# Kernel optimization log

Hardware: AMD Instinct MI355X
Metric: run time of the kernel (lower is better)

## Reference

```python
import jax, jax.numpy as jnp
import numpy as np
from jax import lax

B, C, L, H = 32, 256, 1280, 5
D = L // H  # head dim = 256
EPS = 1e-5


def setup_inputs() -> dict:
    key = jax.random.key(0)
    ks = jax.random.split(key, 16)
    s = 0.02
    inp = {
        "x": jax.random.normal(ks[0], (B, C, L), jnp.float32),
        # rank encoder Linear(L, L)
        "re_w": jax.random.normal(ks[1], (L, L), jnp.float32) * s,
        "re_b": jnp.zeros((L,), jnp.float32),
        # layer norms
        "ln1_g": jnp.ones((L,), jnp.float32), "ln1_b": jnp.zeros((L,), jnp.float32),
        "ln2_g": jnp.ones((L,), jnp.float32), "ln2_b": jnp.zeros((L,), jnp.float32),
        # attention projections (stored [in, out]; y @ W + b)
        "wq": jax.random.normal(ks[2], (L, L), jnp.float32) * s, "bq": jnp.zeros((L,), jnp.float32),
        "wk": jax.random.normal(ks[3], (L, L), jnp.float32) * s, "bk": jnp.zeros((L,), jnp.float32),
        "wv": jax.random.normal(ks[4], (L, L), jnp.float32) * s, "bv": jnp.zeros((L,), jnp.float32),
        "wo": jax.random.normal(ks[5], (L, L), jnp.float32) * s, "bo": jnp.zeros((L,), jnp.float32),
        # FFN (ffn_size == hidden_size == L in this module)
        "ffn_w1": jax.random.normal(ks[6], (L, L), jnp.float32) * s, "ffn_b1": jnp.zeros((L,), jnp.float32),
        "ffn_w2": jax.random.normal(ks[7], (L, L), jnp.float32) * s, "ffn_b2": jnp.zeros((L,), jnp.float32),
        # Conv1d(C, C, k=3, stride=1, pad=1, bias=False) + BatchNorm1d (eval) + ReLU
        "conv_w": jax.random.normal(ks[8], (C, C, 3), jnp.float32) * (2.0 / (C * 3)) ** 0.5,
        "bn_g": jnp.ones((C,), jnp.float32), "bn_b": jnp.zeros((C,), jnp.float32),
        "bn_m": jnp.zeros((C,), jnp.float32), "bn_v": jnp.ones((C,), jnp.float32),
    }
    return inp


def _layernorm(t, g, b):
    m = jnp.mean(t, axis=-1, keepdims=True)
    v = jnp.var(t, axis=-1, keepdims=True)
    return (t - m) * lax.rsqrt(v + EPS) * g + b


def reference(x, re_w, re_b, ln1_g, ln1_b, ln2_g, ln2_b,
              wq, bq, wk, bk, wv, bv, wo, bo,
              ffn_w1, ffn_b1, ffn_w2, ffn_b2,
              conv_w, bn_g, bn_b, bn_m, bn_v):
    b_, c_, l_ = x.shape
    # _getrank_: rank from double argsort (descending), mapped to (L - rank)/L
    rank_i = jnp.argsort(jnp.argsort(-x, axis=-1), axis=-1)
    rank = (l_ - rank_i).astype(x.dtype) / l_
    node = x + rank @ re_w + re_b                      # [B, C, L]

    # EncoderLayer: pre-LN MHSA (attn_bias is None in this call path)
    y = _layernorm(node, ln1_g, ln1_b)
    scale = D ** -0.5
    q = (y @ wq + bq).reshape(b_, c_, H, D).transpose(0, 2, 1, 3) * scale  # [B,H,C,D]
    k = (y @ wk + bk).reshape(b_, c_, H, D).transpose(0, 2, 1, 3)
    v = (y @ wv + bv).reshape(b_, c_, H, D).transpose(0, 2, 1, 3)
    attn = jax.nn.softmax(jnp.einsum('bhqd,bhkd->bhqk', q, k), axis=-1)   # [B,H,C,C]
    o = jnp.einsum('bhqk,bhkd->bhqd', attn, v)
    o = o.transpose(0, 2, 1, 3).reshape(b_, c_, l_) @ wo + bo
    h = node + o  # dropout is identity in eval

    # FFN sublayer
    y2 = _layernorm(h, ln2_g, ln2_b)
    f = jax.nn.gelu(y2 @ ffn_w1 + ffn_b1, approximate=False) @ ffn_w2 + ffn_b2
    h = h + f                                           # [B, C, L]

    # ConvBNRelu: Conv1d(k=3, s=1, p=1, no bias) -> BN (eval stats) -> ReLU
    conv = lax.conv_general_dilated(h, conv_w, window_strides=(1,),
                                    padding=[(1, 1)],
                                    dimension_numbers=('NCH', 'OIH', 'NCH'))
    bn = (conv - bn_m[None, :, None]) * lax.rsqrt(bn_v[None, :, None] + EPS)
    bn = bn * bn_g[None, :, None] + bn_b[None, :, None]
    return jax.nn.relu(bn)
```

## Files before the change

kernel.cpp:

```cpp
#include <hip/hip_runtime.h>
#include <hip/hip_bf16.h>
#include <stdint.h>

#define L_   1280
#define B_   32
#define C_   256
#define H_   5
#define D_   256
#define BC_  8192
#define EPSV 1e-5f

typedef __attribute__((ext_vector_type(8))) short bf16x8;
typedef __attribute__((ext_vector_type(4))) float f32x4;
typedef __hip_bfloat16 bf16;

__device__ __forceinline__ bf16 f2bf(float v) { return __float2bfloat16(v); }
__device__ __forceinline__ float bf2f(bf16 v) { return __bfloat162float(v); }

#define GLDS16(gptr, lptr)                                                        \
    __builtin_amdgcn_global_load_lds(                                             \
        (const __attribute__((address_space(1))) void*)(gptr),                    \
        (__attribute__((address_space(3))) void*)(lptr), 16, 0, 0)

struct WtArgs { const float* src[7]; bf16* dst[7]; };

__global__ __launch_bounds__(256) void transpose7(WtArgs a) {
    const int mat = blockIdx.z;
    const float* src = a.src[mat];
    bf16* dst = a.dst[mat];
    __shared__ float tile[32][33];
    const int bx = blockIdx.x * 32;
    const int by = blockIdx.y * 32;
    const int tx = threadIdx.x, ty = threadIdx.y;
    #pragma unroll
    for (int r = ty; r < 32; r += 8)
        tile[r][tx] = src[(size_t)(by + r) * L_ + bx + tx];
    __syncthreads();
    #pragma unroll
    for (int r = ty; r < 32; r += 8)
        dst[(size_t)(bx + r) * L_ + by + tx] = f2bf(tile[tx][r]);
}

__global__ __launch_bounds__(256) void prep_conv(const float* cw, const float* g, const float* b,
                                                 const float* m, const float* v,
                                                 bf16* WT, float* sc, float* bi) {
    const int i = blockIdx.x * 256 + threadIdx.x;
    if (i < 3 * 256 * 256) {
        const int co = i / 768;
        const int r = i - co * 768;
        const int t = r >> 8, ci = r & 255;
        WT[i] = f2bf(cw[(co * 256 + ci) * 3 + t]);
    }
    if (i < 256) {
        const float s = g[i] * rsqrtf(v[i] + EPSV);
        sc[i] = s;
        bi[i] = b[i] - m[i] * s;
    }
}

__global__ __launch_bounds__(256) void rank_kernel(const float* __restrict__ x, bf16* __restrict__ R) {
    __shared__ float vals[L_];
    __shared__ float sv[L_];
    __shared__ int hist[256];
    __shared__ int pfx[256];
    __shared__ int cur[256];
    const int row = blockIdx.x, tid = threadIdx.x;
    const float* src = x + (size_t)row * L_;
    for (int i = tid; i < L_; i += 256) vals[i] = src[i];
    hist[tid] = 0;
    __syncthreads();
    float myv[5]; int myb[5];
    #pragma unroll
    for (int ii = 0; ii < 5; ii++) {
        const float v = vals[tid + ii * 256];
        int bk = (int)((4.0f - v) * 32.0f);
        bk = bk < 0 ? 0 : (bk > 255 ? 255 : bk);
        myv[ii] = v; myb[ii] = bk;
        atomicAdd(&hist[bk], 1);
    }
    __syncthreads();
    pfx[tid] = hist[tid];
    __syncthreads();
    for (int off = 1; off < 256; off <<= 1) {
        int t = (tid >= off) ? pfx[tid - off] : 0;
        __syncthreads();
        pfx[tid] += t;
        __syncthreads();
    }
    cur[tid] = pfx[tid] - hist[tid];
    __syncthreads();
    #pragma unroll
    for (int ii = 0; ii < 5; ii++) {
        const int pos = atomicAdd(&cur[myb[ii]], 1);
        sv[pos] = myv[ii];
    }
    __syncthreads();
    #pragma unroll
    for (int ii = 0; ii < 5; ii++) {
        const int bk = myb[ii]; const float v = myv[ii];
        const int s = pfx[bk] - hist[bk], e = pfx[bk];
        int cg = s;
        for (int p = s; p < e; p++) cg += (sv[p] > v) ? 1 : 0;
        R[(size_t)row * L_ + tid + ii * 256] = f2bf((float)(L_ - cg) * (1.0f / L_));
    }
}

__global__ __launch_bounds__(256) void ln_kernel(const bf16* __restrict__ in,
                                                 const float* __restrict__ g,
                                                 const float* __restrict__ b,
                                                 bf16* __restrict__ out) {
    const int row = blockIdx.x, tid = threadIdx.x;
    const bf16* src = in + (size_t)row * L_;
    uint2 ra = ((const uint2*)src)[tid];
    bf16 a4[4]; *(uint2*)a4 = ra;
    const float a0 = bf2f(a4[0]), a1 = bf2f(a4[1]), a2 = bf2f(a4[2]), a3 = bf2f(a4[3]);
    float s = a0 + a1 + a2 + a3;
    float ss = a0 * a0 + a1 * a1 + a2 * a2 + a3 * a3;
    float b0 = 0, b1 = 0, b2 = 0, b3 = 0;
    if (tid < 64) {
        uint2 rb = ((const uint2*)src)[256 + tid];
        bf16 b4[4]; *(uint2*)b4 = rb;
        b0 = bf2f(b4[0]); b1 = bf2f(b4[1]); b2 = bf2f(b4[2]); b3 = bf2f(b4[3]);
        s += b0 + b1 + b2 + b3;
        ss += b0 * b0 + b1 * b1 + b2 * b2 + b3 * b3;
    }
    #pragma unroll
    for (int off = 32; off > 0; off >>= 1) {
        s += __shfl_down(s, off, 64);
        ss += __shfl_down(ss, off, 64);
    }
    __shared__ float rs[4], rss[4];
    __shared__ float mean_s, rstd_s;
    if ((tid & 63) == 0) { rs[tid >> 6] = s; rss[tid >> 6] = ss; }
    __syncthreads();
    if (tid == 0) {
        const float S = rs[0] + rs[1] + rs[2] + rs[3];
        const float SS = rss[0] + rss[1] + rss[2] + rss[3];
        const float m = S * (1.0f / L_);
        const float var = SS * (1.0f / L_) - m * m;
        mean_s = m; rstd_s = rsqrtf(var + EPSV);
    }
    __syncthreads();
    const float m = mean_s, r = rstd_s;
    {
        const int c = tid * 4;
        bf16 t4[4];
        t4[0] = f2bf((a0 - m) * r * g[c + 0] + b[c + 0]);
        t4[1] = f2bf((a1 - m) * r * g[c + 1] + b[c + 1]);
        t4[2] = f2bf((a2 - m) * r * g[c + 2] + b[c + 2]);
        t4[3] = f2bf((a3 - m) * r * g[c + 3] + b[c + 3]);
        *(uint2*)(out + (size_t)row * L_ + c) = *(uint2*)t4;
    }
    if (tid < 64) {
        const int c = 1024 + tid * 4;
        bf16 t4[4];
        t4[0] = f2bf((b0 - m) * r * g[c + 0] + b[c + 0]);
        t4[1] = f2bf((b1 - m) * r * g[c + 1] + b[c + 1]);
        t4[2] = f2bf((b2 - m) * r * g[c + 2] + b[c + 2]);
        t4[3] = f2bf((b3 - m) * r * g[c + 3] + b[c + 3]);
        *(uint2*)(out + (size_t)row * L_ + c) = *(uint2*)t4;
    }
}

__global__ __launch_bounds__(256) void softmax_kernel(const bf16* __restrict__ S, bf16* __restrict__ P) {
    const int row = blockIdx.x * 4 + (threadIdx.x >> 6);
    const int l = threadIdx.x & 63;
    const bf16* src = S + (size_t)row * 256 + l * 4;
    uint2 raw = *(const uint2*)src;
    bf16 s4[4]; *(uint2*)s4 = raw;
    float v0 = bf2f(s4[0]), v1 = bf2f(s4[1]);
    float v2 = bf2f(s4[2]), v3 = bf2f(s4[3]);
    float mx = fmaxf(fmaxf(v0, v1), fmaxf(v2, v3));
    #pragma unroll
    for (int off = 1; off < 64; off <<= 1) mx = fmaxf(mx, __shfl_xor(mx, off, 64));
    const float e0 = expf(v0 - mx), e1 = expf(v1 - mx), e2 = expf(v2 - mx), e3 = expf(v3 - mx);
    float sm = e0 + e1 + e2 + e3;
    #pragma unroll
    for (int off = 1; off < 64; off <<= 1) sm += __shfl_xor(sm, off, 64);
    const float inv = 1.0f / sm;
    bf16 t4[4] = { f2bf(e0 * inv), f2bf(e1 * inv), f2bf(e2 * inv), f2bf(e3 * inv) };
    *(uint2*)(P + (size_t)row * 256 + l * 4) = *(uint2*)t4;
}

__global__ __launch_bounds__(256) void zero_pads(bf16* h2T) {
    const int i = blockIdx.x * 256 + threadIdx.x;
    const int b = i >> 9;
    const int which = (i >> 8) & 1;
    const int ci = i & 255;
    const long row = which ? 1281 : 0;
    h2T[(long)b * (1282 * 256) + row * 256 + ci] = f2bf(0.0f);
}

struct GemmP {
    const bf16* A;  long lda, sA1, sA2;
    const bf16* Bt; long ldb, sB1, sB2;
    int zmod;
    int K;
    float* outF; bf16* outB; bf16* outB2; bf16* outB3; long ldc, sC1, sC2;
    const float* bias; const float* bias2; const float* bias3;
    const float* res; const bf16* resB; long ldres, sR1, sR2;
    const float* rowscale; const float* rowbias;
    float scale;
};

constexpr int E_NODE = 0;
constexpr int E_HRES = 1;
constexpr int E_BF16 = 5;
constexpr int E_GELU = 6;
constexpr int E_FFN2T = 7;
constexpr int E_CONVBNR = 8;
constexpr int E_QKV = 9;

template <int EPI>
__global__ __launch_bounds__(256) void gemm_bt(GemmP p) {
    const int nwg  = gridDim.x * gridDim.y * gridDim.z;
    const int orig = (blockIdx.z * gridDim.y + blockIdx.y) * gridDim.x + blockIdx.x;
    int bx, rowg;
    if ((nwg & 7) == 0) {
        const int chunk = nwg >> 3;
        const int xcd = orig & 7, pos = orig >> 3;
        const int rpc = chunk / gridDim.x;
        if (rpc * gridDim.x == chunk) {
            bx   = pos / rpc;
            rowg = xcd * rpc + (pos - bx * rpc);
        } else {
            const int wgid = xcd * chunk + pos;
            bx = wgid % gridDim.x; rowg = wgid / gridDim.x;
        }
    } else {
        bx = blockIdx.x; rowg = blockIdx.z * gridDim.y + blockIdx.y;
    }
    const int by = rowg % gridDim.y;
    const int bz = rowg / gridDim.y;

    const int zq = bz / p.zmod, zr = bz % p.zmod;
    const bf16* A  = p.A  + (long)zq * p.sA1 + (long)zr * p.sA2;
    const bf16* Bt = p.Bt + (long)zq * p.sB1 + (long)zr * p.sB2;
    const int row0 = by * 128, col0 = bx * 128;

    __shared__ __align__(16) bf16 shm[24576];

    const int tid = threadIdx.x;
    const int l = tid & 63, w = tid >> 6;
    const int wr = w >> 1, wc = w & 1;

    f32x4 acc[4][4];
    #pragma unroll
    for (int m = 0; m < 4; m++)
        #pragma unroll
        for (int n = 0; n < 4; n++)
            acc[m][n] = (f32x4){0.f, 0.f, 0.f, 0.f};

    const bf16* gA = A  + (long)(row0 + w * 16 + (l >> 2)) * p.lda + (l & 3) * 8;
    const bf16* gB = Bt + (long)(col0 + w * 16 + (l >> 2)) * p.ldb + (l & 3) * 8;
    const long aStep = 64 * p.lda, bStep = 64 * p.ldb;

    auto STAGE = [&](int buf) {
        bf16* lA = shm + buf * 4096;
        bf16* lB = shm + 12288 + buf * 4096;
        GLDS16(gA,         lA + w * 512);
        GLDS16(gA + aStep, lA + 2048 + w * 512);
        GLDS16(gB,         lB + w * 512);
        GLDS16(gB + bStep, lB + 2048 + w * 512);
        gA += 32; gB += 32;
    };
    auto COMPUTE = [&](int buf) {
        const bf16* lA = shm + buf * 4096;
        const bf16* lB = shm + 12288 + buf * 4096;
        bf16x8 aF[4], bF[4];
        #pragma unroll
        for (int m = 0; m < 4; m++)
            aF[m] = *(const bf16x8*)(lA + (wr * 64 + m * 16 + (l & 15)) * 32 + (l >> 4) * 8);
        #pragma unroll
        for (int n = 0; n < 4; n++)
            bF[n] = *(const bf16x8*)(lB + (wc * 64 + n * 16 + (l & 15)) * 32 + (l >> 4) * 8);
        #pragma unroll
        for (int m = 0; m < 4; m++)
            #pragma unroll
            for (int n = 0; n < 4; n++)
                acc[m][n] = __builtin_amdgcn_mfma_f32_16x16x32_bf16(aF[m], bF[n], acc[m][n], 0, 0, 0);
    };

    const int nt = p.K >> 5;
    STAGE(0); STAGE(1);
    int cb = 0, sb = 2;
    for (int t = 0; t < nt - 1; ++t) {
        asm volatile("s_waitcnt vmcnt(4)" ::: "memory");
        __builtin_amdgcn_sched_barrier(0);
        __builtin_amdgcn_s_barrier();
        if (t + 2 < nt) STAGE(sb);
        COMPUTE(cb);
        cb = (cb == 2) ? 0 : cb + 1;
        sb = (sb == 2) ? 0 : sb + 1;
    }
    asm volatile("s_waitcnt vmcnt(0)" ::: "memory");
    __builtin_amdgcn_sched_barrier(0);
    __builtin_amdgcn_s_barrier();
    COMPUTE(cb);

    if constexpr (EPI == E_QKV) {
        if (col0 >= 2560) {
            const int v0  = col0 - 2560;
            const int hh  = v0 >> 8;
            const int dd0 = v0 & 255;
            const int b_  = row0 >> 8;
            const int c0b = row0 & 255;
            __syncthreads();
            #pragma unroll
            for (int m = 0; m < 4; m++)
                #pragma unroll
                for (int n = 0; n < 4; n++) {
                    const int cc = wc * 64 + n * 16 + (l & 15);
                    const float bb = p.bias3[v0 + cc];
                    #pragma unroll
                    for (int j = 0; j < 4; j++) {
                        const int r = wr * 64 + m * 16 + (l >> 4) * 4 + j;
                        shm[cc * 128 + (r ^ ((cc & 7) << 3))] = f2bf(acc[m][n][j] + bb);
                    }
                }
            __syncthreads();
            const int d = tid >> 1, ch = (tid & 1) * 64;
            bf16* dstRow = p.outB3 +
                (((long)((b_ * H_ + hh) * 256 + dd0 + d)) << 8) + c0b;
            #pragma unroll
            for (int g = 0; g < 8; g++) {
                const int rb = ch + g * 8;
                *(bf16x8*)(dstRow + rb) =
                    *(const bf16x8*)&shm[d * 128 + (rb ^ ((d & 7) << 3))];
            }
            return;
        }
    }

    const long cz = (long)zq * p.sC1 + (long)zr * p.sC2;
    const long rz = (long)zq * p.sR1 + (long)zr * p.sR2;
    #pragma unroll
    for (int m = 0; m < 4; m++) {
        #pragma unroll
        for (int n = 0; n < 4; n++) {
            const int gcol = col0 + wc * 64 + n * 16 + (l & 15);
            #pragma unroll
            for (int j = 0; j < 4; j++) {
                const int grow = row0 + wr * 64 + m * 16 + (l >> 4) * 4 + j;
                const float v = acc[m][n][j];
                if constexpr (EPI == E_NODE) {
                    p.outB[cz + (long)grow * p.ldc + gcol] =
                        f2bf(v + p.bias[gcol] + p.res[rz + (long)grow * p.ldres + gcol]);
                } else if constexpr (EPI == E_HRES) {
                    p.outB[cz + (long)grow * p.ldc + gcol] =
                        f2bf(v + p.bias[gcol] + bf2f(p.resB[rz + (long)grow * p.ldres + gcol]));
                } else if constexpr (EPI == E_BF16) {
                    p.outB[cz + (long)grow * p.ldc + gcol] = f2bf(v);
                } else if constexpr (EPI == E_GELU) {
                    const float t = v + p.bias[gcol];
                    p.outB[cz + (long)grow * p.ldc + gcol] =
                        f2bf(0.5f * t * (1.0f + erff(t * 0.70710678f)));
                } else if constexpr (EPI == E_FFN2T) {
                    const float t = v + p.bias[gcol] +
                                    bf2f(p.resB[rz + (long)grow * p.ldres + gcol]);
                    const int b_ = grow >> 8, ci = grow & 255;
                    p.outB[(long)b_ * (1282 * 256) + (long)(gcol + 1) * 256 + ci] = f2bf(t);
                } else if constexpr (EPI == E_CONVBNR) {
                    const float t = v * p.rowscale[grow] + p.rowbias[grow];
                    p.outF[cz + (long)grow * p.ldc + gcol] = fmaxf(t, 0.0f);
                } else if constexpr (EPI == E_QKV) {
                    if (gcol < 1280) {
                        p.outB[(long)grow * L_ + gcol] = f2bf((v + p.bias[gcol]) * p.scale);
                    } else {
                        const int c2 = gcol - 1280;
                        p.outB2[(long)grow * L_ + c2] = f2bf(v + p.bias2[c2]);
                    }
                }
            }
        }
    }
}

extern "C" void kernel_launch(void* const* d_in, const int* in_sizes, int n_in,
                              void* d_out, int out_size, void* d_ws, size_t ws_size,
                              hipStream_t stream) {
    const float* x    = (const float*)d_in[0];
    const float* re_w = (const float*)d_in[1];
    const float* re_b = (const float*)d_in[2];
    const float* ln1g = (const float*)d_in[3];
    const float* ln1b = (const float*)d_in[4];
    const float* ln2g = (const float*)d_in[5];
    const float* ln2b = (const float*)d_in[6];
    const float* wq   = (const float*)d_in[7];
    const float* bq   = (const float*)d_in[8];
    const float* wk   = (const float*)d_in[9];
    const float* bk   = (const float*)d_in[10];
    const float* wv   = (const float*)d_in[11];
    const float* bv   = (const float*)d_in[12];
    const float* wo   = (const float*)d_in[13];
    const float* bo   = (const float*)d_in[14];
    const float* fw1  = (const float*)d_in[15];
    const float* fb1  = (const float*)d_in[16];
    const float* fw2  = (const float*)d_in[17];
    const float* fb2  = (const float*)d_in[18];
    const float* convw = (const float*)d_in[19];
    const float* bng  = (const float*)d_in[20];
    const float* bnb  = (const float*)d_in[21];
    const float* bnm  = (const float*)d_in[22];
    const float* bnv  = (const float*)d_in[23];
    float* out = (float*)d_out;

    char* ws = (char*)d_ws;
    const size_t SZ_WT     = (size_t)L_ * L_ * 2;
    const size_t SZ_ACT_BF = (size_t)BC_ * L_ * 2;
    const size_t SZ_H2T    = (size_t)B_ * 1282 * 256 * 2;
    const size_t SZ_S      = (size_t)160 * 256 * 256 * 4;

    size_t off = 0;
    bf16* Wt[7];
    for (int i = 0; i < 7; i++) { Wt[i] = (bf16*)(ws + off); off += SZ_WT; }
    bf16* WconvT   = (bf16*)(ws + off); off += 393216;
    float* bnscale = (float*)(ws + off); off += 1024;
    float* bnbias  = (float*)(ws + off); off += 1024;
    bf16* RP  = (bf16*)(ws + off); off += SZ_ACT_BF;
    bf16* Yb  = (bf16*)(ws + off); off += SZ_ACT_BF;
    bf16* Qb  = (bf16*)(ws + off); off += SZ_ACT_BF;
    bf16* Kb  = (bf16*)(ws + off); off += SZ_H2T;
    float* Sb = (float*)(ws + off); off += SZ_S;
    bf16* nodeB = (bf16*)(ws + off); off += SZ_ACT_BF;
    bf16* Sbf = (bf16*)Sb;
    bf16* VT  = Sbf + (size_t)160 * 65536;
    (void)in_sizes; (void)n_in; (void)out_size;

    if (ws_size < off) return;

    WtArgs wa;
    wa.src[0] = re_w; wa.src[1] = wq; wa.src[2] = wk; wa.src[3] = wv;
    wa.src[4] = wo;  wa.src[5] = fw1; wa.src[6] = fw2;
    for (int i = 0; i < 7; i++) wa.dst[i] = Wt[i];
    transpose7<<<dim3(40, 40, 7), dim3(32, 8), 0, stream>>>(wa);
    prep_conv<<<dim3(768), 256, 0, stream>>>(convw, bng, bnb, bnm, bnv, WconvT, bnscale, bnbias);

    rank_kernel<<<dim3(BC_), 256, 0, stream>>>(x, RP);

    const dim3 gBig(L_ / 128, BC_ / 128, 1);
    const dim3 gQKV(3840 / 128, BC_ / 128, 1);
    const dim3 gAttn(2, 2, 160);
    const dim3 blk(256);

    {
        GemmP p{}; p.zmod = 1; p.K = L_;
        p.A = RP; p.lda = L_; p.Bt = Wt[0]; p.ldb = L_;
        p.outB = nodeB; p.ldc = L_; p.bias = re_b; p.res = x; p.ldres = L_;
        gemm_bt<E_NODE><<<gBig, blk, 0, stream>>>(p);
    }
    ln_kernel<<<dim3(BC_), blk, 0, stream>>>(nodeB, ln1g, ln1b, Yb);
    {
        GemmP p{}; p.zmod = 1; p.K = L_;
        p.A = Yb; p.lda = L_; p.Bt = Wt[1]; p.ldb = L_;
        p.outB = Qb; p.outB2 = Kb; p.outB3 = VT;
        p.bias = bq; p.bias2 = bk; p.bias3 = bv; p.scale = 0.0625f;
        gemm_bt<E_QKV><<<gQKV, blk, 0, stream>>>(p);
    }
    {
        GemmP p{}; p.zmod = H_; p.K = 256;
        p.A = Qb;  p.lda = L_; p.sA1 = (long)C_ * L_; p.sA2 = 256;
        p.Bt = Kb; p.ldb = L_; p.sB1 = (long)C_ * L_; p.sB2 = 256;
        p.outB = Sbf; p.ldc = 256; p.sC1 = (long)H_ * 65536; p.sC2 = 65536;
        gemm_bt<E_BF16><<<gAttn, blk, 0, stream>>>(p);
    }
    softmax_kernel<<<dim3(160 * 256 / 4), blk, 0, stream>>>(Sbf, RP);
    {
        GemmP p{}; p.zmod = H_; p.K = 256;
        p.A = RP;  p.lda = 256; p.sA1 = (long)H_ * 65536; p.sA2 = 65536;
        p.Bt = VT; p.ldb = 256; p.sB1 = (long)H_ * 65536; p.sB2 = 65536;
        p.outB = Qb; p.ldc = L_; p.sC1 = (long)C_ * L_; p.sC2 = 256;
        gemm_bt<E_BF16><<<gAttn, blk, 0, stream>>>(p);
    }
    {
        GemmP p{}; p.zmod = 1; p.K = L_;
        p.A = Qb; p.lda = L_; p.Bt = Wt[4]; p.ldb = L_;
        p.outB = nodeB; p.ldc = L_; p.bias = bo; p.resB = nodeB; p.ldres = L_;
        gemm_bt<E_HRES><<<gBig, blk, 0, stream>>>(p);
    }
    ln_kernel<<<dim3(BC_), blk, 0, stream>>>(nodeB, ln2g, ln2b, RP);
    {
        GemmP p{}; p.zmod = 1; p.K = L_;
        p.A = RP; p.lda = L_; p.Bt = Wt[5]; p.ldb = L_;
        p.outB = Yb; p.ldc = L_; p.bias = fb1;
        gemm_bt<E_GELU><<<gBig, blk, 0, stream>>>(p);
    }
    zero_pads<<<dim3(64), blk, 0, stream>>>(Kb);
    {
        GemmP p{}; p.zmod = 1; p.K = L_;
        p.A = Yb; p.lda = L_; p.Bt = Wt[6]; p.ldb = L_;
        p.outB = Kb; p.bias = fb2; p.resB = nodeB; p.ldres = L_;
        gemm_bt<E_FFN2T><<<gBig, blk, 0, stream>>>(p);
    }
    {
        GemmP p{}; p.zmod = 1; p.K = 768;
        p.A = WconvT; p.lda = 768;
        p.Bt = Kb; p.ldb = 256; p.sB1 = 1282 * 256;
        p.outF = out; p.ldc = L_; p.sC1 = (long)C_ * L_;
        p.rowscale = bnscale; p.rowbias = bnbias;
        gemm_bt<E_CONVBNR><<<dim3(L_ / 128, 2, B_), blk, 0, stream>>>(p);
    }
}
```

Baseline: 520.4 us.

## Enlarge GEMM tile to 256x128 and write V-transpose directly from registers

Doubles the M dimension of the shared GEMM block tile from 128 to 256 rows, with each wave now computing 128x64. This raises arithmetic intensity and halves the B-operand reloads, and the grids for all launches are halved in y to match. The LDS-staged transposed V epilogue is replaced with direct 8-byte stores from accumulators, removing a shared-memory round trip at the cost of less coalesced writes. The change doubles accumulator registers and raises LDS use, which may lower occupancy, and it halves the block count, which may under-fill the CUs on smaller launches such as attention and conv.

```diff
diff --git a/kernel.cpp b/kernel.cpp
--- a/kernel.cpp
+++ b/kernel.cpp
@@ -236,46 +236,47 @@
     const int zq = bz / p.zmod, zr = bz % p.zmod;
     const bf16* A  = p.A  + (long)zq * p.sA1 + (long)zr * p.sA2;
     const bf16* Bt = p.Bt + (long)zq * p.sB1 + (long)zr * p.sB2;
-    const int row0 = by * 128, col0 = bx * 128;
-
-    __shared__ __align__(16) bf16 shm[24576];
+    const int row0 = by * 256, col0 = bx * 128;
+
+    __shared__ __align__(16) bf16 shm[36864];
 
     const int tid = threadIdx.x;
     const int l = tid & 63, w = tid >> 6;
     const int wr = w >> 1, wc = w & 1;
 
-    f32x4 acc[4][4];
-    #pragma unroll
-    for (int m = 0; m < 4; m++)
+    f32x4 acc[8][4];
+    #pragma unroll
+    for (int m = 0; m < 8; m++)
         #pragma unroll
         for (int n = 0; n < 4; n++)
             acc[m][n] = (f32x4){0.f, 0.f, 0.f, 0.f};
 
     const bf16* gA = A  + (long)(row0 + w * 16 + (l >> 2)) * p.lda + (l & 3) * 8;
     const bf16* gB = Bt + (long)(col0 + w * 16 + (l >> 2)) * p.ldb + (l & 3) * 8;
-    const long aStep = 64 * p.lda, bStep = 64 * p.ldb;
 
     auto STAGE = [&](int buf) {
-        bf16* lA = shm + buf * 4096;
-        bf16* lB = shm + 12288 + buf * 4096;
-        GLDS16(gA,         lA + w * 512);
-        GLDS16(gA + aStep, lA + 2048 + w * 512);
-        GLDS16(gB,         lB + w * 512);
-        GLDS16(gB + bStep, lB + 2048 + w * 512);
+        bf16* lA = shm + buf * 8192;
+        bf16* lB = shm + 24576 + buf * 4096;
+        GLDS16(gA,                 lA + w * 512);
+        GLDS16(gA +  64 * p.lda,   lA + 2048 + w * 512);
+        GLDS16(gA + 128 * p.lda,   lA + 4096 + w * 512);
+        GLDS16(gA + 192 * p.lda,   lA + 6144 + w * 512);
+        GLDS16(gB,                 lB + w * 512);
+        GLDS16(gB +  64 * p.ldb,   lB + 2048 + w * 512);
         gA += 32; gB += 32;
     };
     auto COMPUTE = [&](int buf) {
-        const bf16* lA = shm + buf * 4096;
-        const bf16* lB = shm + 12288 + buf * 4096;
-        bf16x8 aF[4], bF[4];
+        const bf16* lA = shm + buf * 8192;
+        const bf16* lB = shm + 24576 + buf * 4096;
+        bf16x8 aF[8], bF[4];
         #pragma unroll
-        for (int m = 0; m < 4; m++)
-            aF[m] = *(const bf16x8*)(lA + (wr * 64 + m * 16 + (l & 15)) * 32 + (l >> 4) * 8);
+        for (int m = 0; m < 8; m++)
+            aF[m] = *(const bf16x8*)(lA + (wr * 128 + m * 16 + (l & 15)) * 32 + (l >> 4) * 8);
         #pragma unroll
         for (int n = 0; n < 4; n++)
             bF[n] = *(const bf16x8*)(lB + (wc * 64 + n * 16 + (l & 15)) * 32 + (l >> 4) * 8);
         #pragma unroll
-        for (int m = 0; m < 4; m++)
+        for (int m = 0; m < 8; m++)
             #pragma unroll
             for (int n = 0; n < 4; n++)
                 acc[m][n] = __builtin_amdgcn_mfma_f32_16x16x32_bf16(aF[m], bF[n], acc[m][n], 0, 0, 0);
@@ -285,7 +286,7 @@
     STAGE(0); STAGE(1);
     int cb = 0, sb = 2;
     for (int t = 0; t < nt - 1; ++t) {
-        asm volatile("s_waitcnt vmcnt(4)" ::: "memory");
+        asm volatile("s_waitcnt vmcnt(6)" ::: "memory");
         __builtin_amdgcn_sched_barrier(0);
         __builtin_amdgcn_s_barrier();
         if (t + 2 < nt) STAGE(sb);
@@ -298,50 +299,31 @@
     __builtin_amdgcn_s_barrier();
     COMPUTE(cb);
 
-    if constexpr (EPI == E_QKV) {
-        if (col0 >= 2560) {
-            const int v0  = col0 - 2560;
-            const int hh  = v0 >> 8;
-            const int dd0 = v0 & 255;
-            const int b_  = row0 >> 8;
-            const int c0b = row0 & 255;
-            __syncthreads();
-            #pragma unroll
-            for (int m = 0; m < 4; m++)
-                #pragma unroll
-                for (int n = 0; n < 4; n++) {
-                    const int cc = wc * 64 + n * 16 + (l & 15);
-                    const float bb = p.bias3[v0 + cc];
-                    #pragma unroll
-                    for (int j = 0; j < 4; j++) {
-                        const int r = wr * 64 + m * 16 + (l >> 4) * 4 + j;
-                        shm[cc * 128 + (r ^ ((cc & 7) << 3))] = f2bf(acc[m][n][j] + bb);
-                    }
-                }
-            __syncthreads();
-            const int d = tid >> 1, ch = (tid & 1) * 64;
-            bf16* dstRow = p.outB3 +
-                (((long)((b_ * H_ + hh) * 256 + dd0 + d)) << 8) + c0b;
-            #pragma unroll
-            for (int g = 0; g < 8; g++) {
-                const int rb = ch + g * 8;
-                *(bf16x8*)(dstRow + rb) =
-                    *(const bf16x8*)&shm[d * 128 + (rb ^ ((d & 7) << 3))];
-            }
-            return;
-        }
-    }
-
     const long cz = (long)zq * p.sC1 + (long)zr * p.sC2;
     const long rz = (long)zq * p.sR1 + (long)zr * p.sR2;
     #pragma unroll
-    for (int m = 0; m < 4; m++) {
+    for (int m = 0; m < 8; m++) {
         #pragma unroll
         for (int n = 0; n < 4; n++) {
             const int gcol = col0 + wc * 64 + n * 16 + (l & 15);
+            if constexpr (EPI == E_QKV) {
+                if (gcol >= 2560) {
+                    const int c3 = gcol - 2560;
+                    const int h_ = c3 >> 8, d_ = c3 & 255;
+                    const int crow = wr * 128 + m * 16 + (l >> 4) * 4;
+                    const int b_ = row0 >> 8;
+                    const float bb = p.bias3[c3];
+                    bf16 t4[4];
+                    #pragma unroll
+                    for (int j = 0; j < 4; j++) t4[j] = f2bf(acc[m][n][j] + bb);
+                    *(uint2*)(p.outB3 + (((long)((b_ * H_ + h_) * 256 + d_)) << 8) + crow) =
+                        *(uint2*)t4;
+                    continue;
+                }
+            }
             #pragma unroll
             for (int j = 0; j < 4; j++) {
-                const int grow = row0 + wr * 64 + m * 16 + (l >> 4) * 4 + j;
+                const int grow = row0 + wr * 128 + m * 16 + (l >> 4) * 4 + j;
                 const float v = acc[m][n][j];
                 if constexpr (EPI == E_NODE) {
                     p.outB[cz + (long)grow * p.ldc + gcol] =
@@ -438,9 +420,9 @@
 
     rank_kernel<<<dim3(BC_), 256, 0, stream>>>(x, RP);
 
-    const dim3 gBig(L_ / 128, BC_ / 128, 1);
-    const dim3 gQKV(3840 / 128, BC_ / 128, 1);
-    const dim3 gAttn(2, 2, 160);
+    const dim3 gBig(L_ / 128, BC_ / 256, 1);
+    const dim3 gQKV(3840 / 128, BC_ / 256, 1);
+    const dim3 gAttn(2, 1, 160);
     const dim3 blk(256);
 
     {
@@ -498,6 +480,6 @@
         p.Bt = Kb; p.ldb = 256; p.sB1 = 1282 * 256;
         p.outF = out; p.ldc = L_; p.sC1 = (long)C_ * L_;
         p.rowscale = bnscale; p.rowbias = bnbias;
-        gemm_bt<E_CONVBNR><<<dim3(L_ / 128, 2, B_), blk, 0, stream>>>(p);
-    }
-}
+        gemm_bt<E_CONVBNR><<<dim3(L_ / 128, 1, B_), blk, 0, stream>>>(p);
+    }
+}
```

Measured after the change: 580.6 us. 1.12x slower.
